# Kernel optimization log

Measured on AMD Instinct MI355X. Metric: run time of the kernel, lower is better.

## Reference

```python
import jax, jax.numpy as jnp
import numpy as np

RADIUS = 0.2
NSAMPLE = 32


def setup_inputs() -> dict:
    key = jax.random.key(0)
    k1, k2 = jax.random.split(key)
    B, N = 8, 4096
    xyz = jax.random.uniform(k1, (B, N, 3), dtype=jnp.float32)
    xyz_new = jax.random.uniform(k2, (B, N, 3), dtype=jnp.float32)  # ignored by forward, kept for signature fidelity
    return {"xyz": xyz, "xyz_new": xyz_new}


def _ball_query(radius, nsample, xyz, new_xyz):
    # xyz: [B, N, 3] source points; new_xyz: [B, M, 3] query centers.
    # Returns idx: [B, M, nsample] int32, matching pointnet2 CUDA ball_query:
    # first `nsample` indices j (in increasing j order) with ||q - p_j||^2 < r^2;
    # unused slots are filled with the first valid index.
    B, N, _ = xyz.shape
    sq_src = jnp.sum(xyz * xyz, axis=-1)          # [B, N]
    sq_q = jnp.sum(new_xyz * new_xyz, axis=-1)    # [B, M]
    # d2[b, m, n] = ||q_m - p_n||^2
    d2 = sq_q[:, :, None] + sq_src[:, None, :] - 2.0 * jnp.einsum(
        "bmc,bnc->bmn", new_xyz, xyz)             # [B, M, N]
    mask = d2 < (radius * radius)                 # [B, M, N] bool
    # key = index j when within radius, else sentinel N (sorts to the end)
    idx_range = jnp.arange(N, dtype=jnp.int32)
    keys = jnp.where(mask, idx_range[None, None, :], jnp.int32(N))
    sorted_keys = jnp.sort(keys, axis=-1)[..., :nsample]  # [B, M, nsample]
    first = sorted_keys[..., 0:1]                 # first valid index (pad value)
    idx = jnp.where(sorted_keys < N, sorted_keys, first)
    return idx.astype(jnp.int32)


def reference(xyz, xyz_new):
    # Faithful to the module: ball_query(radius, nsample, xyz, xyz) — xyz_new unused.
    return _ball_query(RADIUS, NSAMPLE, xyz, xyz)
```

## Files before the change

kernel.cpp:

```cpp
#include <hip/hip_runtime.h>
#include <cstdint>


#define BQ_N   4096
#define BQ_B   8
#define BQ_NS  32
#define BQ_R2  0.04f

__device__ __forceinline__ float sq_plain(float x, float y, float z) {
    float r, t;
    asm("v_mul_f32 %0, %2, %2\n\t"
        "v_mul_f32 %1, %3, %3\n\t"
        "v_add_f32 %0, %0, %1\n\t"
        "v_mul_f32 %1, %4, %4\n\t"
        "v_add_f32 %0, %0, %1"
        : "=&v"(r), "=&v"(t)
        : "v"(x), "v"(y), "v"(z));
    return r;
}

__device__ __forceinline__ float d2_mixed(float qx, float qy, float qz, float sqq,
                                          float sx, float sy, float sz, float sqs) {
    float r, t;
    asm("v_mul_f32 %0, %2, %5\n\t"
        "v_fma_f32 %0, %3, %6, %0\n\t"
        "v_fma_f32 %0, %4, %7, %0\n\t"
        "v_add_f32 %0, %0, %0\n\t"
        "v_add_f32 %1, %8, %9\n\t"
        "v_sub_f32 %0, %1, %0"
        : "=&v"(r), "=&v"(t)
        : "v"(qx), "v"(qy), "v"(qz), "v"(sx), "v"(sy), "v"(sz),
          "v"(sqq), "v"(sqs));
    return r;
}

__global__ __launch_bounds__(256, 2)
void ball_query_kernel(const float* __restrict__ xyz, int* __restrict__ out)
{
    __shared__ float4 pts[BQ_N];

    const int b     = blockIdx.x >> 6;
    const int qbase = (blockIdx.x & 63) << 6;
    const float* __restrict__ src = xyz + (size_t)b * BQ_N * 3;

    for (int j = threadIdx.x; j < BQ_N; j += 256) {
        const float x = src[3 * j + 0];
        const float y = src[3 * j + 1];
        const float z = src[3 * j + 2];
        pts[j] = make_float4(x, y, z, sq_plain(x, y, z));
    }
    __syncthreads();

    const int lane = threadIdx.x & 63;
    const int wid  = threadIdx.x >> 6;
    int* __restrict__ outb = out + (size_t)(b * BQ_N) * BQ_NS;

    for (int qi = 0; qi < 16; ++qi) {
        const int m = qbase + (wid << 4) + qi;
        const float4 q = pts[m];
        const float sqq = q.w;

        uint64_t word = 0;
        int found = 0;
        for (int c = 0; c < 8; ++c) {
            #pragma unroll
            for (int u = 0; u < 8; ++u) {
                const int k = c * 8 + u;
                const float4 s = pts[(k << 6) + lane];
                const float d2 = d2_mixed(q.x, q.y, q.z, sqq,
                                          s.x, s.y, s.z, s.w);
                const uint64_t bal = __ballot(d2 < BQ_R2);
                if (lane == k) word = bal;
                found += __popcll(bal);
            }
            if (found >= BQ_NS) break;
        }

        const int cnt = __popcll(word);
        int incl = cnt;
        #pragma unroll
        for (int off = 1; off < 64; off <<= 1) {
            const int t = __shfl_up(incl, off);
            if (lane >= off) incl += t;
        }
        const int pre   = incl - cnt;
        const int total = __shfl(incl, 63);

        int first;
        const uint64_t nz = __ballot(word != 0ull);
        if (nz == 0ull) {
            first = BQ_N;
        } else {
            const int fl = __builtin_ctzll(nz);
            const uint64_t fw = __shfl(word, fl);
            first = (fl << 6) + __builtin_ctzll(fw);
        }

        int* __restrict__ orow = outb + m * BQ_NS;
        uint64_t w = word;
        int pos = pre;
        while (w != 0ull && pos < BQ_NS) {
            const int bit = __builtin_ctzll(w);
            orow[pos] = (lane << 6) + bit;
            w &= (w - 1);
            ++pos;
        }
        if (lane == 0) {
            for (int p = total; p < BQ_NS; ++p) orow[p] = first;
        }
    }
}

extern "C" void kernel_launch(void* const* d_in, const int* in_sizes, int n_in,
                              void* d_out, int out_size, void* d_ws, size_t ws_size,
                              hipStream_t stream)
{
    const float* xyz = (const float*)d_in[0];
    int* out = (int*)d_out;
    hipLaunchKernelGGL(ball_query_kernel, dim3(BQ_B * 64), dim3(256), 0, stream,
                       xyz, out);
}
```

Measured before the change: 90.94 us.

## Process eight queries per wavefront jointly, reusing each shared-memory point load

Each wavefront now holds eight query points in registers and streams the source points once, testing every loaded point against all still-active queries. A query stops being tested once it has found enough neighbours. The block grows to 512 threads, so each wave handles eight queries instead of sixteen. Padding writes are also spread across lanes instead of a serial loop in lane 0. This cuts repeated LDS reads and the serial per-query loop, at the cost of more registers, per-query branching on the active mask, and coarser early exit, since the scan continues in 256-point steps until all eight queries are done.

```diff
diff --git a/kernel.cpp b/kernel.cpp
--- a/kernel.cpp
+++ b/kernel.cpp
@@ -34,7 +34,39 @@
     return r;
 }
 
-__global__ __launch_bounds__(256, 2)
+__device__ __forceinline__ void emit_query(int* orow, int lane, uint64_t word) {
+    const int cnt = __popcll(word);
+    int incl = cnt;
+    #pragma unroll
+    for (int off = 1; off < 64; off <<= 1) {
+        const int t = __shfl_up(incl, off);
+        if (lane >= off) incl += t;
+    }
+    const int pre   = incl - cnt;
+    const int total = __shfl(incl, 63);
+
+    int first;
+    const uint64_t nz = __ballot(word != 0ull);
+    if (nz == 0ull) {
+        first = BQ_N;
+    } else {
+        const int fl = __builtin_ctzll(nz);
+        const uint64_t fw = __shfl(word, fl);
+        first = (fl << 6) + __builtin_ctzll(fw);
+    }
+
+    uint64_t w = word;
+    int pos = pre;
+    while (w != 0ull && pos < BQ_NS) {
+        const int bit = __builtin_ctzll(w);
+        orow[pos] = (lane << 6) + bit;
+        w &= (w - 1);
+        ++pos;
+    }
+    if (lane >= total && lane < BQ_NS) orow[lane] = first;
+}
+
+__global__ __launch_bounds__(512, 4)
 void ball_query_kernel(const float* __restrict__ xyz, int* __restrict__ out)
 {
     __shared__ float4 pts[BQ_N];
@@ -42,8 +74,11 @@
     const int b     = blockIdx.x >> 6;
     const int qbase = (blockIdx.x & 63) << 6;
     const float* __restrict__ src = xyz + (size_t)b * BQ_N * 3;
+    const int lane = threadIdx.x & 63;
+    const int wid  = threadIdx.x >> 6;
+    int* __restrict__ outb = out + (size_t)(b * BQ_N) * BQ_NS;
 
-    for (int j = threadIdx.x; j < BQ_N; j += 256) {
+    for (int j = threadIdx.x; j < BQ_N; j += 512) {
         const float x = src[3 * j + 0];
         const float y = src[3 * j + 1];
         const float z = src[3 * j + 2];
@@ -51,63 +86,40 @@
     }
     __syncthreads();
 
-    const int lane = threadIdx.x & 63;
-    const int wid  = threadIdx.x >> 6;
-    int* __restrict__ outb = out + (size_t)(b * BQ_N) * BQ_NS;
+    float4 Q[8];
+    #pragma unroll
+    for (int j = 0; j < 8; ++j) Q[j] = pts[qbase + (wid << 3) + j];
 
-    for (int qi = 0; qi < 16; ++qi) {
-        const int m = qbase + (wid << 4) + qi;
-        const float4 q = pts[m];
-        const float sqq = q.w;
+    uint64_t W[8] = {0, 0, 0, 0, 0, 0, 0, 0};
+    int      F[8] = {0, 0, 0, 0, 0, 0, 0, 0};
+    unsigned active = 0xFFu;
 
-        uint64_t word = 0;
-        int found = 0;
-        for (int c = 0; c < 8; ++c) {
+    #pragma unroll 1
+    for (int c = 0; c < 16 && active; ++c) {
+        #pragma unroll
+        for (int u = 0; u < 4; ++u) {
+            const int k = (c << 2) + u;
+            const float4 s = pts[(k << 6) + lane];
             #pragma unroll
-            for (int u = 0; u < 8; ++u) {
-                const int k = c * 8 + u;
-                const float4 s = pts[(k << 6) + lane];
-                const float d2 = d2_mixed(q.x, q.y, q.z, sqq,
-                                          s.x, s.y, s.z, s.w);
-                const uint64_t bal = __ballot(d2 < BQ_R2);
-                if (lane == k) word = bal;
-                found += __popcll(bal);
+            for (int i = 0; i < 8; ++i) {
+                if (active & (1u << i)) {
+                    const float d2 = d2_mixed(Q[i].x, Q[i].y, Q[i].z, Q[i].w,
+                                              s.x, s.y, s.z, s.w);
+                    const uint64_t bal = __ballot(d2 < BQ_R2);
+                    if (lane == k) W[i] = bal;
+                    F[i] += (int)__popcll(bal);
+                }
             }
-            if (found >= BQ_NS) break;
         }
+        #pragma unroll
+        for (int i = 0; i < 8; ++i)
+            if (F[i] >= BQ_NS) active &= ~(1u << i);
+    }
 
-        const int cnt = __popcll(word);
-        int incl = cnt;
-        #pragma unroll
-        for (int off = 1; off < 64; off <<= 1) {
-            const int t = __shfl_up(incl, off);
-            if (lane >= off) incl += t;
-        }
-        const int pre   = incl - cnt;
-        const int total = __shfl(incl, 63);
-
-        int first;
-        const uint64_t nz = __ballot(word != 0ull);
-        if (nz == 0ull) {
-            first = BQ_N;
-        } else {
-            const int fl = __builtin_ctzll(nz);
-            const uint64_t fw = __shfl(word, fl);
-            first = (fl << 6) + __builtin_ctzll(fw);
-        }
-
-        int* __restrict__ orow = outb + m * BQ_NS;
-        uint64_t w = word;
-        int pos = pre;
-        while (w != 0ull && pos < BQ_NS) {
-            const int bit = __builtin_ctzll(w);
-            orow[pos] = (lane << 6) + bit;
-            w &= (w - 1);
-            ++pos;
-        }
-        if (lane == 0) {
-            for (int p = total; p < BQ_NS; ++p) orow[p] = first;
-        }
+    #pragma unroll 1
+    for (int j = 0; j < 8; ++j) {
+        const int m = qbase + (wid << 3) + j;
+        emit_query(outb + (size_t)m * BQ_NS, lane, W[j]);
     }
 }
 
@@ -117,6 +129,6 @@
 {
     const float* xyz = (const float*)d_in[0];
     int* out = (int*)d_out;
-    hipLaunchKernelGGL(ball_query_kernel, dim3(BQ_B * 64), dim3(256), 0, stream,
+    hipLaunchKernelGGL(ball_query_kernel, dim3(BQ_B * 64), dim3(512), 0, stream,
                        xyz, out);
 }
```

Result: faster. 85.85 us (-5.6%).
